# Kernel tuning notes

Measured on AMD Instinct MI355X. Metric: run time of the kernel, lower is better.

## Reference

```python
import jax, jax.numpy as jnp
import numpy as np
import math

N_EMBD = 768
N_HEAD = 12
B, T = 4, 1024


def setup_inputs() -> dict:
    key = jax.random.key(0)
    ks = jax.random.split(key, 12)
    s = 0.02
    d = N_EMBD
    inp = {
        'x': jax.random.normal(ks[0], (B, T, d), dtype=jnp.float32),
        'refractory_state': jax.random.uniform(ks[1], (B, T), dtype=jnp.float32),
        'ln1_w': jnp.ones((d,), jnp.float32),
        'ln1_b': jnp.zeros((d,), jnp.float32),
        'c_attn_w': jax.random.normal(ks[2], (d, 3 * d), dtype=jnp.float32) * s,
        'c_attn_b': jnp.zeros((3 * d,), jnp.float32),
        'c_proj_w': jax.random.normal(ks[3], (d, d), dtype=jnp.float32) * s,
        'c_proj_b': jnp.zeros((d,), jnp.float32),
        'threshold': jnp.full((N_HEAD,), 0.01, jnp.float32),
        'leak': jnp.full((N_HEAD,), 2.0, jnp.float32),
        'steepness': jnp.full((N_HEAD,), 2.0, jnp.float32),
        'refractory_strength': jnp.full((N_HEAD,), -2.0, jnp.float32),
        'cross_layer_weight': jnp.full((N_HEAD,), -2.0, jnp.float32),
        'ln2_w': jnp.ones((d,), jnp.float32),
        'ln2_b': jnp.zeros((d,), jnp.float32),
        'fc_w': jax.random.normal(ks[4], (d, 4 * d), dtype=jnp.float32) * s,
        'fc_b': jnp.zeros((4 * d,), jnp.float32),
        'proj_w': jax.random.normal(ks[5], (4 * d, d), dtype=jnp.float32) * s,
        'proj_b': jnp.zeros((d,), jnp.float32),
    }
    return inp


def _layer_norm(x, w, b, eps=1e-5):
    m = jnp.mean(x, axis=-1, keepdims=True)
    v = jnp.var(x, axis=-1, keepdims=True)
    return (x - m) * jax.lax.rsqrt(v + eps) * w + b


def _per_head(p):
    # [H] -> [1, H, 1, 1]
    return p.reshape(1, -1, 1, 1)


def ember_block(x, refractory_state, ln1_w, ln1_b, c_attn_w, c_attn_b,
                c_proj_w, c_proj_b, threshold, leak, steepness,
                refractory_strength, cross_layer_weight,
                ln2_w, ln2_b, fc_w, fc_b, proj_w, proj_b):
    Bx, Tx, C = x.shape
    hd = C // N_HEAD

    h = _layer_norm(x, ln1_w, ln1_b)
    qkv = h @ c_attn_w + c_attn_b
    q, k, v = jnp.split(qkv, 3, axis=-1)
    # [B, T, C] -> [B, H, T, hd]
    q = q.reshape(Bx, Tx, N_HEAD, hd).transpose(0, 2, 1, 3)
    k = k.reshape(Bx, Tx, N_HEAD, hd).transpose(0, 2, 1, 3)
    v = v.reshape(Bx, Tx, N_HEAD, hd).transpose(0, 2, 1, 3)

    att = jnp.einsum('bhqd,bhkd->bhqk', q, k) * (1.0 / math.sqrt(hd))
    causal = jnp.tril(jnp.ones((Tx, Tx), dtype=bool))
    att = jnp.where(causal, att, -jnp.inf)
    att_probs = jax.nn.softmax(att, axis=-1)

    # per-head LIF modulation with refractory dynamics
    thr = jnp.abs(_per_head(threshold)) * 0.1
    lk = jax.nn.sigmoid(_per_head(leak))
    stp = jax.nn.softplus(_per_head(steepness))

    column_load = att_probs.mean(axis=-2, keepdims=True)  # [B,H,1,T]
    ref_strength = jax.nn.softplus(_per_head(refractory_strength))
    eff_thr = thr + ref_strength * column_load
    cross_w = jax.nn.sigmoid(_per_head(cross_layer_weight))
    prev_load = refractory_state[:, None, None, :]  # [B,1,1,T]
    eff_thr = eff_thr + cross_w * prev_load

    fire_mask = jax.nn.sigmoid(stp * (att_probs - eff_thr))
    lif_weights = fire_mask + lk * (1.0 - fire_mask)
    modulated = att_probs * lif_weights
    modulated = modulated / (modulated.sum(axis=-1, keepdims=True) + 1e-8)
    new_refractory = modulated.mean(axis=1).mean(axis=-2)  # [B,T]

    y = jnp.einsum('bhqk,bhkd->bhqd', modulated, v)
    y = y.transpose(0, 2, 1, 3).reshape(Bx, Tx, C)
    y = y @ c_proj_w + c_proj_b
    x = x + y

    # MLP
    h2 = _layer_norm(x, ln2_w, ln2_b)
    h2 = jax.nn.gelu(h2 @ fc_w + fc_b, approximate=False)
    h2 = h2 @ proj_w + proj_b
    x = x + h2
    return x, new_refractory


def reference(x, refractory_state, ln1_w, ln1_b, c_attn_w, c_attn_b,
              c_proj_w, c_proj_b, threshold, leak, steepness,
              refractory_strength, cross_layer_weight,
              ln2_w, ln2_b, fc_w, fc_b, proj_w, proj_b):
    return ember_block(x, refractory_state, ln1_w, ln1_b, c_attn_w, c_attn_b,
                       c_proj_w, c_proj_b, threshold, leak, steepness,
                       refractory_strength, cross_layer_weight,
                       ln2_w, ln2_b, fc_w, fc_b, proj_w, proj_b)
```

## Files before the change

kernel.cpp:

```cpp
#include <hip/hip_runtime.h>
#include <hip/hip_bf16.h>
#include <math.h>

typedef unsigned short ushort;
typedef __attribute__((ext_vector_type(8))) unsigned short ushort8;
typedef __attribute__((ext_vector_type(8))) short s16x8;
typedef __attribute__((ext_vector_type(4))) float f32x4;

constexpr int NE = 768;
constexpr int NH = 12;
constexpr int HD = 64;
constexpr int Bc = 4;
constexpr int Tc = 1024;
constexpr int BT = Bc * Tc;

__device__ __forceinline__ ushort f2bf(float f) {
    __hip_bfloat16 h = __float2bfloat16(f);
    return *reinterpret_cast<ushort*>(&h);
}
__device__ __forceinline__ float bf2f(ushort u) {
    return __uint_as_float(((unsigned)u) << 16);
}
__device__ __forceinline__ float softplus_f(float x) {
    return (x > 20.f) ? x : log1pf(__expf(x));
}
__device__ __forceinline__ float rcp_f(float x) {
#if __has_builtin(__builtin_amdgcn_rcpf)
    return __builtin_amdgcn_rcpf(x);
#else
    return 1.f / x;
#endif
}
__device__ __forceinline__ void gload16(const void* g, void* l) {
    __builtin_amdgcn_global_load_lds((const __attribute__((address_space(1))) void*)g,
                                     (__attribute__((address_space(3))) void*)l, 16, 0, 0);
}

__global__ __launch_bounds__(256) void ln_kernel(const float* __restrict__ x,
                                                 const float* __restrict__ w,
                                                 const float* __restrict__ b,
                                                 ushort* __restrict__ out) {
    int row = blockIdx.x;
    const float* xr = x + (size_t)row * NE;
    int t = threadIdx.x;
    float v0 = xr[t], v1 = xr[t + 256], v2 = xr[t + 512];
    __shared__ float red[256], red2[256];
    red[t] = v0 + v1 + v2;
    red2[t] = v0 * v0 + v1 * v1 + v2 * v2;
    __syncthreads();
    for (int o = 128; o > 0; o >>= 1) {
        if (t < o) { red[t] += red[t + o]; red2[t] += red2[t + o]; }
        __syncthreads();
    }
    float mean = red[0] * (1.0f / NE);
    float var = red2[0] * (1.0f / NE) - mean * mean;
    float rs = rsqrtf(var + 1e-5f);
    ushort* orow = out + (size_t)row * NE;
    orow[t]       = f2bf((v0 - mean) * rs * w[t]       + b[t]);
    orow[t + 256] = f2bf((v1 - mean) * rs * w[t + 256] + b[t + 256]);
    orow[t + 512] = f2bf((v2 - mean) * rs * w[t + 512] + b[t + 512]);
}

__global__ __launch_bounds__(256) void wconvert(const float* __restrict__ W,
                                                ushort* __restrict__ Wt, int K, int N) {
    __shared__ float t[32][33];
    int n0 = blockIdx.x * 32, k0 = blockIdx.y * 32;
    int c = threadIdx.x & 31, r4 = threadIdx.x >> 5;
#pragma unroll
    for (int i = 0; i < 4; ++i) {
        int r = r4 + i * 8;
        t[r][c] = W[(size_t)(k0 + r) * N + n0 + c];
    }
    __syncthreads();
#pragma unroll
    for (int i = 0; i < 4; ++i) {
        int r = r4 + i * 8;
        Wt[(size_t)(n0 + r) * K + k0 + c] = f2bf(t[c][r]);
    }
}

template <int BM, int BN, int OUT_MODE, int ACT, bool RES>
__global__ __launch_bounds__(256) void mfma_gemm(
    const ushort* __restrict__ A, const ushort* __restrict__ Bt,
    const float* __restrict__ bias, const float* __restrict__ residual,
    float* __restrict__ Cf, ushort* __restrict__ Cb,
    ushort* __restrict__ Qo, ushort* __restrict__ Ko, ushort* __restrict__ Vo,
    int M, int N, int K, int NBX) {
    constexpr int NF = (BM == 128) ? 4 : 2;
    constexpr int MF = (BM == 64 && BN == 64) ? 2 : 4;
    constexpr int WN = BN / (NF * 16);
    constexpr int APASS = BM / 32, BPASS = BN / 32;
    __shared__ __align__(16) ushort As[BM * 64];
    __shared__ __align__(16) ushort Bs[BN * 64];
    int tid = threadIdx.x;
    int lane = tid & 63;
    int nb = gridDim.x;
    int lin = blockIdx.x;
    int nl = (lin & 7) * (nb >> 3) + (lin >> 3);
    int bx = nl % NBX, by = nl / NBX;
    int m0 = by * BM, n0 = bx * BN;
    int wave = tid >> 6;
    int wr = wave / WN, wc = wave % WN;
    f32x4 acc[MF][NF] = {};
    int srow = tid >> 3;
    int scol = (tid & 7) ^ (srow & 7);
    const ushort* ga = A + (size_t)(m0 + srow) * K + scol * 8;
    const ushort* gb = Bt + (size_t)(n0 + srow) * K + scol * 8;
    char* lA = (char*)As + tid * 16;
    char* lB = (char*)Bs + tid * 16;
    int fr = lane & 15, g = lane >> 4;
    unsigned swz = (unsigned)((fr & 7) << 4);
    const char* abase = (const char*)As + (wr * (MF * 16) + fr) * 128;
    const char* bbase = (const char*)Bs + (wc * (NF * 16) + fr) * 128;
    for (int k0 = 0; k0 < K; k0 += 64) {
#pragma unroll
        for (int p = 0; p < APASS; ++p)
            gload16(ga + (size_t)(p * 32) * K + k0, lA + p * 4096);
#pragma unroll
        for (int p = 0; p < BPASS; ++p)
            gload16(gb + (size_t)(p * 32) * K + k0, lB + p * 4096);
        __syncthreads();
#pragma unroll
        for (int ks = 0; ks < 2; ++ks) {
            unsigned o = ((unsigned)(g * 16 + ks * 64)) ^ swz;
            s16x8 af[MF], bf[NF];
#pragma unroll
            for (int i = 0; i < MF; ++i) af[i] = *(const s16x8*)(abase + i * 2048 + o);
#pragma unroll
            for (int i = 0; i < NF; ++i) bf[i] = *(const s16x8*)(bbase + i * 2048 + o);
#pragma unroll
            for (int mi = 0; mi < MF; ++mi)
#pragma unroll
                for (int ni = 0; ni < NF; ++ni)
                    acc[mi][ni] = __builtin_amdgcn_mfma_f32_16x16x32_bf16(af[mi], bf[ni], acc[mi][ni], 0, 0, 0);
        }
        __syncthreads();
    }
#pragma unroll
    for (int mi = 0; mi < MF; ++mi) {
#pragma unroll
        for (int ni = 0; ni < NF; ++ni) {
#pragma unroll
            for (int j = 0; j < 4; ++j) {
                int row = m0 + wr * (MF * 16) + mi * 16 + g * 4 + j;
                int col = n0 + wc * (NF * 16) + ni * 16 + fr;
                float v = acc[mi][ni][j] + bias[col];
                if (ACT == 1) v = 0.5f * v * (1.0f + erff(v * 0.70710678118654752f));
                if (RES) v += residual[(size_t)row * N + col];
                if (OUT_MODE == 0) {
                    Cf[(size_t)row * N + col] = v;
                } else if (OUT_MODE == 1) {
                    Cb[(size_t)row * N + col] = f2bf(v);
                } else {
                    int which = col >= 1536 ? 2 : (col >= 768 ? 1 : 0);
                    int rem = col - which * 768;
                    int hh = rem >> 6, d = rem & 63;
                    int b_ = row >> 10, t_ = row & 1023;
                    if (which == 2)
                        Vo[((size_t)(b_ * NH + hh) * HD + d) * Tc + t_] = f2bf(v);
                    else {
                        ushort* dst = which == 0 ? Qo : Ko;
                        dst[((size_t)(b_ * NH + hh) * Tc + t_) * HD + d] = f2bf(v);
                    }
                }
            }
        }
    }
}


__global__ __launch_bounds__(128) void attn_P(
    const ushort* __restrict__ Qp, const ushort* __restrict__ Kp,
    ushort* __restrict__ Pbuf, float* __restrict__ denom, float* __restrict__ colsum) {
    int beta = blockIdx.x;
    int tq = 63 - beta / 48;
    int bh = beta % 48;
    int tid = threadIdx.x;
    int kh = tid >> 6, lane = tid & 63, qlane = lane & 15, g = lane >> 4;
    __shared__ ushort plds[2][16][48];
    __shared__ float cs[1056];
    __shared__ float dden[2][16];
    int nst = (tq + 2) >> 1;
    int smid = (nst + 1) >> 1;
    int slo = kh ? smid : 0, shi = kh ? nst : smid;
    int kmaxc = (tq + 1) * 16;
    for (int i = tid; i < 1056; i += 128) cs[i] = 0.f;
    const ushort* Qb = Qp + (size_t)bh * Tc * HD;
    const ushort* Kb = Kp + (size_t)bh * Tc * HD;
    const ushort* qr = Qb + (size_t)(tq * 16 + qlane) * HD + g * 8;
    s16x8 qf0 = *(const s16x8*)qr;
    s16x8 qf1 = *(const s16x8*)(qr + 32);
    ushort* panel = Pbuf + ((size_t)bh * 1056 + (unsigned)(((tq + 1) * (tq + 1)) >> 2)) * 512;
    int q = tq * 16 + qlane;
    float dpart = 0.f;
    for (int s = slo; s < shi; ++s) {
        int kt0 = 2 * s, kt1 = 2 * s + 1;
        {
            const ushort* kr = Kb + (size_t)(kt0 * 16 + qlane) * HD + g * 8;
            s16x8 kf0 = *(const s16x8*)kr;
            s16x8 kf1 = *(const s16x8*)(kr + 32);
            f32x4 z = {0.f, 0.f, 0.f, 0.f};
            z = __builtin_amdgcn_mfma_f32_16x16x32_bf16(kf0, qf0, z, 0, 0, 0);
            z = __builtin_amdgcn_mfma_f32_16x16x32_bf16(kf1, qf1, z, 0, 0, 0);
#pragma unroll
            for (int j = 0; j < 4; ++j) {
                int key = kt0 * 16 + g * 4 + j;
                float p = (key <= q) ? __expf(z[j] * 0.125f - 8.f) : 0.f;
                dpart += p;
                plds[kh][qlane][g * 4 + j] = f2bf(p);
            }
        }
        if (kt1 <= tq) {
            const ushort* kr = Kb + (size_t)(kt1 * 16 + qlane) * HD + g * 8;
            s16x8 kf0 = *(const s16x8*)kr;
            s16x8 kf1 = *(const s16x8*)(kr + 32);
            f32x4 z = {0.f, 0.f, 0.f, 0.f};
            z = __builtin_amdgcn_mfma_f32_16x16x32_bf16(kf0, qf0, z, 0, 0, 0);
            z = __builtin_amdgcn_mfma_f32_16x16x32_bf16(kf1, qf1, z, 0, 0, 0);
#pragma unroll
            for (int j = 0; j < 4; ++j) {
                int key = kt1 * 16 + g * 4 + j;
                float p = (key <= q) ? __expf(z[j] * 0.125f - 8.f) : 0.f;
                dpart += p;
                plds[kh][qlane][16 + g * 4 + j] = f2bf(p);
            }
        } else {
#pragma unroll
            for (int j = 0; j < 4; ++j) plds[kh][qlane][16 + g * 4 + j] = 0;
        }
        s16x8 pa = *(const s16x8*)&plds[kh][qlane][g * 8];
        *(s16x8*)(panel + (size_t)s * 512 + lane * 8) = pa;
    }
    dpart += __shfl_xor(dpart, 16);
    dpart += __shfl_xor(dpart, 32);
    if (lane < 16) dden[kh][lane] = dpart;
    __syncthreads();
    float dsum = dden[0][qlane] + dden[1][qlane];
    if (tid < 16) denom[(size_t)bh * Tc + tq * 16 + tid] = dden[0][tid] + dden[1][tid];
    float dinvq = rcp_f(dsum);
    for (int s = slo; s < shi; ++s) {
        s16x8 v8 = *(const s16x8*)(panel + (size_t)s * 512 + lane * 8);
        int k0 = s * 32 + g * 8;
#pragma unroll
        for (int j = 0; j < 8; ++j) {
            float r = bf2f((ushort)v8[j]) * dinvq;
            r += __shfl_xor(r, 1);
            r += __shfl_xor(r, 2);
            r += __shfl_xor(r, 4);
            r += __shfl_xor(r, 8);
            if (qlane == 0) cs[k0 + j] += r;
        }
    }
    __syncthreads();
    for (int i = tid; i < kmaxc; i += 128)
        atomicAdd(&colsum[(size_t)bh * Tc + i], cs[i]);
}

__global__ __launch_bounds__(128) void attn_CD(
    ushort* __restrict__ Pbuf, const ushort* __restrict__ Vt,
    const float* __restrict__ denom, const float* __restrict__ colsum,
    const float* __restrict__ refr_in,
    const float* __restrict__ threshold, const float* __restrict__ leak,
    const float* __restrict__ steepness, const float* __restrict__ refr_strength,
    const float* __restrict__ cross_w,
    ushort* __restrict__ ybuf, float* __restrict__ refr_out) {
    int beta = blockIdx.x;
    int tq = 63 - beta / 48;
    int bh = beta % 48;
    int b = bh / NH, h = bh - b * NH;
    int tid = threadIdx.x;
    int kh = tid >> 6, lane = tid & 63, qlane = lane & 15, g = lane >> 4;
    __shared__ float eff[1056];
    __shared__ float cs[1056];
    __shared__ float msum[2][16];
    __shared__ float minvL[16];
    __shared__ float ymrg[16][68];
    int nst = (tq + 2) >> 1;
    int smid = (nst + 1) >> 1;
    int slo = kh ? smid : 0, shi = kh ? nst : smid;
    int kmaxc = (tq + 1) * 16;
    float thr = fabsf(threshold[h]) * 0.1f;
    float lk = 1.f / (1.f + __expf(-leak[h]));
    float lk1m = 1.f - lk;
    float stp = softplus_f(steepness[h]);
    float rfs = softplus_f(refr_strength[h]);
    float crw = 1.f / (1.f + __expf(-cross_w[h]));
    for (int i = tid; i < 1056; i += 128) {
        eff[i] = (i < kmaxc)
                     ? thr + rfs * (colsum[(size_t)bh * Tc + i] * (1.f / 1024.f))
                           + crw * refr_in[(size_t)b * Tc + i]
                     : 0.f;
        cs[i] = 0.f;
    }
    float dinvq = rcp_f(denom[(size_t)bh * Tc + tq * 16 + qlane]);
    __syncthreads();
    ushort* panel = Pbuf + ((size_t)bh * 1056 + (unsigned)(((tq + 1) * (tq + 1)) >> 2)) * 512;
    float msp = 0.f;
#pragma unroll 2
    for (int s = slo; s < shi; ++s) {
        s16x8 v8 = *(const s16x8*)(panel + (size_t)s * 512 + lane * 8);
        int k0 = s * 32 + g * 8;
        s16x8 pw;
#pragma unroll
        for (int j = 0; j < 8; ++j) {
            float p = bf2f((ushort)v8[j]) * dinvq;
            float fire = rcp_f(1.f + __expf(-stp * (p - eff[k0 + j])));
            float pt = p * (lk + lk1m * fire);
            msp += pt;
            pw[j] = (short)f2bf(pt);
        }
        *(s16x8*)(panel + (size_t)s * 512 + lane * 8) = pw;
    }
    msp += __shfl_xor(msp, 16);
    msp += __shfl_xor(msp, 32);
    if (lane < 16) msum[kh][lane] = msp;
    __syncthreads();
    if (tid < 16) minvL[tid] = rcp_f(msum[0][tid] + msum[1][tid] + 1e-8f);
    __syncthreads();
    float minvq = minvL[qlane];
    const ushort* Vh = Vt + (size_t)bh * HD * Tc;
    f32x4 accY[4] = {};
    for (int s = slo; s < shi; ++s) {
        s16x8 pa = *(const s16x8*)(panel + (size_t)s * 512 + lane * 8);
        int k0 = s * 32 + g * 8;
#pragma unroll
        for (int j = 0; j < 8; ++j) {
            float r = bf2f((ushort)pa[j]) * minvq;
            r += __shfl_xor(r, 1);
            r += __shfl_xor(r, 2);
            r += __shfl_xor(r, 4);
            r += __shfl_xor(r, 8);
            if (qlane == 0) cs[k0 + j] += r;
        }
#pragma unroll
        for (int dt = 0; dt < 4; ++dt) {
            const ushort* vp = Vh + (size_t)(dt * 16 + qlane) * Tc + s * 32 + g * 8;
            s16x8 vf = *(const s16x8*)vp;
            accY[dt] = __builtin_amdgcn_mfma_f32_16x16x32_bf16(pa, vf, accY[dt], 0, 0, 0);
        }
    }
    if (kh == 1) {
#pragma unroll
        for (int dt = 0; dt < 4; ++dt)
#pragma unroll
            for (int j = 0; j < 4; ++j)
                ymrg[g * 4 + j][dt * 16 + qlane] = accY[dt][j];
    }
    __syncthreads();
    if (kh == 0) {
#pragma unroll
        for (int dt = 0; dt < 4; ++dt)
#pragma unroll
            for (int j = 0; j < 4; ++j) {
                float y = (accY[dt][j] + ymrg[g * 4 + j][dt * 16 + qlane]) * minvL[g * 4 + j];
                ybuf[(size_t)(b * Tc + tq * 16 + g * 4 + j) * NE + h * 64 + dt * 16 + qlane] =
                    f2bf(y);
            }
    }
    for (int i = tid; i < kmaxc; i += 128)
        atomicAdd(&refr_out[(size_t)b * Tc + i], cs[i] * (1.f / (NH * Tc)));
}

extern "C" void kernel_launch(void* const* d_in, const int* in_sizes, int n_in,
                              void* d_out, int out_size, void* d_ws, size_t ws_size,
                              hipStream_t stream) {
    const float* x        = (const float*)d_in[0];
    const float* refr     = (const float*)d_in[1];
    const float* ln1_w    = (const float*)d_in[2];
    const float* ln1_b    = (const float*)d_in[3];
    const float* c_attn_w = (const float*)d_in[4];
    const float* c_attn_b = (const float*)d_in[5];
    const float* c_proj_w = (const float*)d_in[6];
    const float* c_proj_b = (const float*)d_in[7];
    const float* threshold = (const float*)d_in[8];
    const float* leak      = (const float*)d_in[9];
    const float* steepness = (const float*)d_in[10];
    const float* refractory_strength = (const float*)d_in[11];
    const float* cross_layer_weight  = (const float*)d_in[12];
    const float* ln2_w    = (const float*)d_in[13];
    const float* ln2_b    = (const float*)d_in[14];
    const float* fc_w     = (const float*)d_in[15];
    const float* fc_b     = (const float*)d_in[16];
    const float* proj_w   = (const float*)d_in[17];
    const float* proj_b   = (const float*)d_in[18];

    char* ws = (char*)d_ws;
    ushort* hbuf   = (ushort*)(ws + 0);
    ushort* qb     = (ushort*)(ws + 6291456);
    ushort* kb     = (ushort*)(ws + 12582912);
    ushort* vtg    = (ushort*)(ws + 18874368);
    ushort* ybuf   = (ushort*)(ws + 25165824);
    ushort* fc_act = (ushort*)(ws + 6291456);
    float*  denomb = (float*)(ws + 31457280);
    float*  colsum = (float*)(ws + 31653888);
    ushort* wt_attn  = (ushort*)(ws + 31850496);
    ushort* wt_cproj = (ushort*)(ws + 35389440);
    ushort* wt_fc    = (ushort*)(ws + 36569088);
    ushort* wt_proj  = (ushort*)(ws + 41287680);
    ushort* Pbuf     = (ushort*)(ws + 46006272);

    float* xout = (float*)d_out;
    float* refr_out = xout + (size_t)BT * NE;

    hipMemsetAsync(colsum, 0, (size_t)Bc * NH * Tc * sizeof(float), stream);
    hipMemsetAsync(refr_out, 0, (size_t)Bc * Tc * sizeof(float), stream);

    wconvert<<<dim3(2304 / 32, 768 / 32), 256, 0, stream>>>(c_attn_w, wt_attn, 768, 2304);
    wconvert<<<dim3(768 / 32, 768 / 32), 256, 0, stream>>>(c_proj_w, wt_cproj, 768, 768);
    wconvert<<<dim3(3072 / 32, 768 / 32), 256, 0, stream>>>(fc_w, wt_fc, 768, 3072);
    wconvert<<<dim3(768 / 32, 3072 / 32), 256, 0, stream>>>(proj_w, wt_proj, 3072, 768);

    ln_kernel<<<BT, 256, 0, stream>>>(x, ln1_w, ln1_b, hbuf);

    mfma_gemm<64, 128, 2, 0, false><<<1152, 256, 0, stream>>>(
        hbuf, wt_attn, c_attn_b, nullptr, nullptr, nullptr, qb, kb, vtg,
        BT, 3 * NE, NE, 18);

    attn_P<<<48 * 64, 128, 0, stream>>>(qb, kb, Pbuf, denomb, colsum);
    attn_CD<<<48 * 64, 128, 0, stream>>>(
        Pbuf, vtg, denomb, colsum, refr, threshold, leak, steepness,
        refractory_strength, cross_layer_weight, ybuf, refr_out);

    mfma_gemm<64, 64, 0, 0, true><<<768, 256, 0, stream>>>(
        ybuf, wt_cproj, c_proj_b, x, xout, nullptr, nullptr, nullptr, nullptr,
        BT, NE, NE, 12);

    ln_kernel<<<BT, 256, 0, stream>>>(xout, ln2_w, ln2_b, hbuf);

    mfma_gemm<128, 128, 1, 1, false><<<768, 256, 0, stream>>>(
        hbuf, wt_fc, fc_b, nullptr, nullptr, fc_act, nullptr, nullptr, nullptr,
        BT, 4 * NE, NE, 24);

    mfma_gemm<64, 64, 0, 0, true><<<768, 256, 0, stream>>>(
        fc_act, wt_proj, proj_b, xout, xout, nullptr, nullptr, nullptr, nullptr,
        BT, NE, 4 * NE, 12);
}
```

Measured before the change: 256.9 us.

## Split attention key range across four waves and recompute modulated probs instead of writeback

Both attention kernels now launch 256 threads and split each query tile's key strips across four wavefronts instead of two, with cross-wave reductions done through shared memory (LDS atomics for the output accumulator). attn_CD no longer writes modulated probabilities back to the global P buffer; it recomputes the sigmoid-weighted values in the second pass, so Pbuf becomes read-only. The aim is more parallelism per tile on the long causal rows and less global write traffic, at the cost of duplicated exp/sigmoid math and LDS atomic contention.

```diff
diff --git a/kernel.cpp b/kernel.cpp
--- a/kernel.cpp
+++ b/kernel.cpp
@@ -169,22 +169,24 @@
 }
 
 
-__global__ __launch_bounds__(128) void attn_P(
+__global__ __launch_bounds__(256) void attn_P(
     const ushort* __restrict__ Qp, const ushort* __restrict__ Kp,
     ushort* __restrict__ Pbuf, float* __restrict__ denom, float* __restrict__ colsum) {
     int beta = blockIdx.x;
     int tq = 63 - beta / 48;
     int bh = beta % 48;
     int tid = threadIdx.x;
-    int kh = tid >> 6, lane = tid & 63, qlane = lane & 15, g = lane >> 4;
-    __shared__ ushort plds[2][16][48];
+    int w = tid >> 6, lane = tid & 63, qlane = lane & 15, g = lane >> 4;
+    __shared__ ushort plds[4][16][48];
     __shared__ float cs[1056];
-    __shared__ float dden[2][16];
+    __shared__ float dden[4][16];
+    __shared__ float dinvL[16];
     int nst = (tq + 2) >> 1;
-    int smid = (nst + 1) >> 1;
-    int slo = kh ? smid : 0, shi = kh ? nst : smid;
+    int base = nst >> 2, rem = nst & 3;
+    int slo = w * base + (w < rem ? w : rem);
+    int shi = slo + base + (w < rem ? 1 : 0);
     int kmaxc = (tq + 1) * 16;
-    for (int i = tid; i < 1056; i += 128) cs[i] = 0.f;
+    for (int i = tid; i < 1056; i += 256) cs[i] = 0.f;
     const ushort* Qb = Qp + (size_t)bh * Tc * HD;
     const ushort* Kb = Kp + (size_t)bh * Tc * HD;
     const ushort* qr = Qb + (size_t)(tq * 16 + qlane) * HD + g * 8;
@@ -207,7 +209,7 @@
                 int key = kt0 * 16 + g * 4 + j;
                 float p = (key <= q) ? __expf(z[j] * 0.125f - 8.f) : 0.f;
                 dpart += p;
-                plds[kh][qlane][g * 4 + j] = f2bf(p);
+                plds[w][qlane][g * 4 + j] = f2bf(p);
             }
         }
         if (kt1 <= tq) {
@@ -222,22 +224,26 @@
                 int key = kt1 * 16 + g * 4 + j;
                 float p = (key <= q) ? __expf(z[j] * 0.125f - 8.f) : 0.f;
                 dpart += p;
-                plds[kh][qlane][16 + g * 4 + j] = f2bf(p);
+                plds[w][qlane][16 + g * 4 + j] = f2bf(p);
             }
         } else {
 #pragma unroll
-            for (int j = 0; j < 4; ++j) plds[kh][qlane][16 + g * 4 + j] = 0;
-        }
-        s16x8 pa = *(const s16x8*)&plds[kh][qlane][g * 8];
+            for (int j = 0; j < 4; ++j) plds[w][qlane][16 + g * 4 + j] = 0;
+        }
+        s16x8 pa = *(const s16x8*)&plds[w][qlane][g * 8];
         *(s16x8*)(panel + (size_t)s * 512 + lane * 8) = pa;
     }
     dpart += __shfl_xor(dpart, 16);
     dpart += __shfl_xor(dpart, 32);
-    if (lane < 16) dden[kh][lane] = dpart;
-    __syncthreads();
-    float dsum = dden[0][qlane] + dden[1][qlane];
-    if (tid < 16) denom[(size_t)bh * Tc + tq * 16 + tid] = dden[0][tid] + dden[1][tid];
-    float dinvq = rcp_f(dsum);
+    if (lane < 16) dden[w][lane] = dpart;
+    __syncthreads();
+    if (tid < 16) {
+        float d = dden[0][tid] + dden[1][tid] + dden[2][tid] + dden[3][tid];
+        denom[(size_t)bh * Tc + tq * 16 + tid] = d;
+        dinvL[tid] = rcp_f(d);
+    }
+    __syncthreads();
+    float dinvq = dinvL[qlane];
     for (int s = slo; s < shi; ++s) {
         s16x8 v8 = *(const s16x8*)(panel + (size_t)s * 512 + lane * 8);
         int k0 = s * 32 + g * 8;
@@ -252,12 +258,12 @@
         }
     }
     __syncthreads();
-    for (int i = tid; i < kmaxc; i += 128)
+    for (int i = tid; i < kmaxc; i += 256)
         atomicAdd(&colsum[(size_t)bh * Tc + i], cs[i]);
 }
 
-__global__ __launch_bounds__(128) void attn_CD(
-    ushort* __restrict__ Pbuf, const ushort* __restrict__ Vt,
+__global__ __launch_bounds__(256) void attn_CD(
+    const ushort* __restrict__ Pbuf, const ushort* __restrict__ Vt,
     const float* __restrict__ denom, const float* __restrict__ colsum,
     const float* __restrict__ refr_in,
     const float* __restrict__ threshold, const float* __restrict__ leak,
@@ -269,15 +275,16 @@
     int bh = beta % 48;
     int b = bh / NH, h = bh - b * NH;
     int tid = threadIdx.x;
-    int kh = tid >> 6, lane = tid & 63, qlane = lane & 15, g = lane >> 4;
+    int w = tid >> 6, lane = tid & 63, qlane = lane & 15, g = lane >> 4;
     __shared__ float eff[1056];
     __shared__ float cs[1056];
-    __shared__ float msum[2][16];
+    __shared__ float msum[4][16];
     __shared__ float minvL[16];
-    __shared__ float ymrg[16][68];
+    __shared__ float ylds[16][64];
     int nst = (tq + 2) >> 1;
-    int smid = (nst + 1) >> 1;
-    int slo = kh ? smid : 0, shi = kh ? nst : smid;
+    int base = nst >> 2, rem = nst & 3;
+    int slo = w * base + (w < rem ? w : rem);
+    int shi = slo + base + (w < rem ? 1 : 0);
     int kmaxc = (tq + 1) * 16;
     float thr = fabsf(threshold[h]) * 0.1f;
     float lk = 1.f / (1.f + __expf(-leak[h]));
@@ -285,47 +292,51 @@
     float stp = softplus_f(steepness[h]);
     float rfs = softplus_f(refr_strength[h]);
     float crw = 1.f / (1.f + __expf(-cross_w[h]));
-    for (int i = tid; i < 1056; i += 128) {
+    for (int i = tid; i < 1056; i += 256) {
         eff[i] = (i < kmaxc)
                      ? thr + rfs * (colsum[(size_t)bh * Tc + i] * (1.f / 1024.f))
                            + crw * refr_in[(size_t)b * Tc + i]
                      : 0.f;
         cs[i] = 0.f;
     }
+    for (int i = tid; i < 1024; i += 256) ((float*)ylds)[i] = 0.f;
     float dinvq = rcp_f(denom[(size_t)bh * Tc + tq * 16 + qlane]);
     __syncthreads();
-    ushort* panel = Pbuf + ((size_t)bh * 1056 + (unsigned)(((tq + 1) * (tq + 1)) >> 2)) * 512;
+    const ushort* panel =
+        Pbuf + ((size_t)bh * 1056 + (unsigned)(((tq + 1) * (tq + 1)) >> 2)) * 512;
     float msp = 0.f;
 #pragma unroll 2
     for (int s = slo; s < shi; ++s) {
         s16x8 v8 = *(const s16x8*)(panel + (size_t)s * 512 + lane * 8);
         int k0 = s * 32 + g * 8;
-        s16x8 pw;
+#pragma unroll
+        for (int j = 0; j < 8; ++j) {
+            float p = bf2f((ushort)v8[j]) * dinvq;
+            float fire = rcp_f(1.f + __expf(-stp * (p - eff[k0 + j])));
+            msp += p * (lk + lk1m * fire);
+        }
+    }
+    msp += __shfl_xor(msp, 16);
+    msp += __shfl_xor(msp, 32);
+    if (lane < 16) msum[w][lane] = msp;
+    __syncthreads();
+    if (tid < 16)
+        minvL[tid] = rcp_f(msum[0][tid] + msum[1][tid] + msum[2][tid] + msum[3][tid] + 1e-8f);
+    __syncthreads();
+    float minvq = minvL[qlane];
+    const ushort* Vh = Vt + (size_t)bh * HD * Tc;
+    f32x4 accY[4] = {};
+    for (int s = slo; s < shi; ++s) {
+        s16x8 v8 = *(const s16x8*)(panel + (size_t)s * 512 + lane * 8);
+        int k0 = s * 32 + g * 8;
+        s16x8 pa;
 #pragma unroll
         for (int j = 0; j < 8; ++j) {
             float p = bf2f((ushort)v8[j]) * dinvq;
             float fire = rcp_f(1.f + __expf(-stp * (p - eff[k0 + j])));
             float pt = p * (lk + lk1m * fire);
-            msp += pt;
-            pw[j] = (short)f2bf(pt);
-        }
-        *(s16x8*)(panel + (size_t)s * 512 + lane * 8) = pw;
-    }
-    msp += __shfl_xor(msp, 16);
-    msp += __shfl_xor(msp, 32);
-    if (lane < 16) msum[kh][lane] = msp;
-    __syncthreads();
-    if (tid < 16) minvL[tid] = rcp_f(msum[0][tid] + msum[1][tid] + 1e-8f);
-    __syncthreads();
-    float minvq = minvL[qlane];
-    const ushort* Vh = Vt + (size_t)bh * HD * Tc;
-    f32x4 accY[4] = {};
-    for (int s = slo; s < shi; ++s) {
-        s16x8 pa = *(const s16x8*)(panel + (size_t)s * 512 + lane * 8);
-        int k0 = s * 32 + g * 8;
-#pragma unroll
-        for (int j = 0; j < 8; ++j) {
-            float r = bf2f((ushort)pa[j]) * minvq;
+            pa[j] = (short)f2bf(pt);
+            float r = pt * minvq;
             r += __shfl_xor(r, 1);
             r += __shfl_xor(r, 2);
             r += __shfl_xor(r, 4);
@@ -339,25 +350,18 @@
             accY[dt] = __builtin_amdgcn_mfma_f32_16x16x32_bf16(pa, vf, accY[dt], 0, 0, 0);
         }
     }
-    if (kh == 1) {
-#pragma unroll
-        for (int dt = 0; dt < 4; ++dt)
-#pragma unroll
-            for (int j = 0; j < 4; ++j)
-                ymrg[g * 4 + j][dt * 16 + qlane] = accY[dt][j];
-    }
-    __syncthreads();
-    if (kh == 0) {
-#pragma unroll
-        for (int dt = 0; dt < 4; ++dt)
-#pragma unroll
-            for (int j = 0; j < 4; ++j) {
-                float y = (accY[dt][j] + ymrg[g * 4 + j][dt * 16 + qlane]) * minvL[g * 4 + j];
-                ybuf[(size_t)(b * Tc + tq * 16 + g * 4 + j) * NE + h * 64 + dt * 16 + qlane] =
-                    f2bf(y);
-            }
-    }
-    for (int i = tid; i < kmaxc; i += 128)
+#pragma unroll
+    for (int dt = 0; dt < 4; ++dt)
+#pragma unroll
+        for (int j = 0; j < 4; ++j)
+            atomicAdd(&ylds[g * 4 + j][dt * 16 + qlane], accY[dt][j]);
+    __syncthreads();
+    for (int i = tid; i < 1024; i += 256) {
+        int qq = i >> 6, dd = i & 63;
+        ybuf[(size_t)(b * Tc + tq * 16 + qq) * NE + h * 64 + dd] =
+            f2bf(ylds[qq][dd] * minvL[qq]);
+    }
+    for (int i = tid; i < kmaxc; i += 256)
         atomicAdd(&refr_out[(size_t)b * Tc + i], cs[i] * (1.f / (NH * Tc)));
 }
 
@@ -416,8 +420,8 @@
         hbuf, wt_attn, c_attn_b, nullptr, nullptr, nullptr, qb, kb, vtg,
         BT, 3 * NE, NE, 18);
 
-    attn_P<<<48 * 64, 128, 0, stream>>>(qb, kb, Pbuf, denomb, colsum);
-    attn_CD<<<48 * 64, 128, 0, stream>>>(
+    attn_P<<<48 * 64, 256, 0, stream>>>(qb, kb, Pbuf, denomb, colsum);
+    attn_CD<<<48 * 64, 256, 0, stream>>>(
         Pbuf, vtg, denomb, colsum, refr, threshold, leak, steepness,
         refractory_strength, cross_layer_weight, ybuf, refr_out);
 
```

New measurement: 297.0 us. 15.6% more time.
